# Kernel tuning notes

Measured on AMD Instinct MI355X. Metric: run time of the kernel, lower is better.

Reference implementation:

```python
import jax, jax.numpy as jnp
import numpy as np

B, LD, LP = 32, 512, 4096
DRUG_VOCAB, PROT_VOCAB, H = 600, 26, 128


def setup_inputs() -> dict:
    key = jax.random.key(0)
    ks = jax.random.split(key, 8)
    drug_ids = jax.random.randint(ks[0], (B, LD), 0, DRUG_VOCAB)
    prot_ids = jax.random.randint(ks[1], (B, LP), 0, PROT_VOCAB)
    drug_emb = jax.random.normal(ks[2], (DRUG_VOCAB, H), dtype=jnp.float32) * 0.02
    prot_emb = jax.random.normal(ks[3], (PROT_VOCAB, H), dtype=jnp.float32) * 0.02
    # classifier: Linear(2H -> 64), ReLU, Linear(64 -> 1); stored as [in, out]
    W1 = jax.random.normal(ks[4], (2 * H, 64), dtype=jnp.float32) * (1.0 / np.sqrt(2 * H))
    b1 = jnp.zeros((64,), dtype=jnp.float32)
    W2 = jax.random.normal(ks[5], (64, 1), dtype=jnp.float32) * (1.0 / np.sqrt(64))
    b2 = jnp.zeros((1,), dtype=jnp.float32)
    return {"drug_ids": drug_ids, "prot_ids": prot_ids,
            "drug_emb": drug_emb, "prot_emb": prot_emb,
            "W1": W1, "b1": b1, "W2": W2, "b2": b2}


def reference(drug_ids, prot_ids, drug_emb, prot_emb, W1, b1, W2, b2):
    d_feat = drug_emb[drug_ids]                      # [B, LD, H]
    p_feat = prot_emb[prot_ids]                      # [B, LP, H]
    aff = jnp.einsum('bld,bmd->blm', d_feat, p_feat) # [B, LD, LP]
    att_d = jax.nn.softmax(aff.max(axis=2), axis=1)[..., None]  # [B, LD, 1]
    att_p = jax.nn.softmax(aff.max(axis=1), axis=1)[..., None]  # [B, LP, 1]
    d_vec = (d_feat * att_d).sum(axis=1)             # [B, H]
    p_vec = (p_feat * att_p).sum(axis=1)             # [B, H]
    combined = jnp.concatenate([d_vec, p_vec], axis=1)  # [B, 2H]
    h = jax.nn.relu(combined @ W1 + b1)
    return h @ W2 + b2                               # [B, 1]
```

## Files before the change

### kernel.cpp

```cpp
#include <hip/hip_runtime.h>
#include <float.h>
#include <math.h>

#define NB 32
#define LD 512
#define LP 4096
#define HD 128
#define PV 26

__global__ __launch_bounds__(512) void k_scores(const int* __restrict__ drug_ids,
                                                const int* __restrict__ prot_ids,
                                                const float* __restrict__ drug_emb,
                                                const float* __restrict__ prot_emb,
                                                float* __restrict__ rowmax,
                                                float* __restrict__ colpart) {
    int b = blockIdx.x >> 3;
    int chunk = blockIdx.x & 7;
    int t = threadIdx.x;
    int q = __builtin_amdgcn_readfirstlane(t >> 6);
    int lane = t & 63;
    int l = chunk * 64 + lane;

    __shared__ float red[8][64][27];
    __shared__ unsigned wor[8];

    const int4* pid4 = reinterpret_cast<const int4*>(prot_ids + b * LP);
    int4 i0 = pid4[t], i1 = pid4[t + 512];
    unsigned pm = (1u << i0.x) | (1u << i0.y) | (1u << i0.z) | (1u << i0.w)
                | (1u << i1.x) | (1u << i1.y) | (1u << i1.z) | (1u << i1.w);
    #pragma unroll
    for (int off = 32; off; off >>= 1) pm |= __shfl_xor(pm, off, 64);
    if (lane == 0) wor[q] = pm;

    const float* __restrict__ A =
        drug_emb + (size_t)drug_ids[b * LD + l] * HD + q * 16;
    float4 a[4];
    #pragma unroll
    for (int i = 0; i < 4; ++i) a[i] = reinterpret_cast<const float4*>(A)[i];

    const float* __restrict__ Bq = prot_emb + q * 16;
    float s[PV];
    #pragma unroll
    for (int v = 0; v < PV; ++v) s[v] = 0.f;

    #pragma unroll
    for (int i = 0; i < 4; ++i) {
        float4 av = a[i];
        #pragma unroll
        for (int v = 0; v < PV; ++v) {
            float4 p = reinterpret_cast<const float4*>(Bq + v * HD)[i];
            s[v] = fmaf(av.x, p.x, fmaf(av.y, p.y,
                   fmaf(av.z, p.z, fmaf(av.w, p.w, s[v]))));
        }
    }

    #pragma unroll
    for (int v = 0; v < PV; ++v) red[q][lane][v] = s[v];
    __syncthreads();

    unsigned msk = wor[0] | wor[1] | wor[2] | wor[3]
                 | wor[4] | wor[5] | wor[6] | wor[7];

    for (int o = t; o < 64 * PV; o += 512) {
        int l2 = o / PV, v = o - l2 * PV;
        float sum = red[0][l2][v] + red[1][l2][v] + red[2][l2][v] + red[3][l2][v]
                  + red[4][l2][v] + red[5][l2][v] + red[6][l2][v] + red[7][l2][v];
        red[0][l2][v] = sum;
    }
    __syncthreads();

    if (t < 64) {
        float m = -FLT_MAX;
        #pragma unroll
        for (int v = 0; v < PV; ++v)
            if ((msk >> v) & 1) m = fmaxf(m, red[0][t][v]);
        rowmax[b * LD + chunk * 64 + t] = m;
    } else if (t < 64 + PV) {
        int v = t - 64;
        float m = -FLT_MAX;
        for (int r = 0; r < 64; ++r) m = fmaxf(m, red[0][r][v]);
        colpart[((b << 3) + chunk) * 32 + v] = m;
    }
}

__global__ __launch_bounds__(1024) void k_tail(const int* __restrict__ drug_ids,
                                               const int* __restrict__ prot_ids,
                                               const float* __restrict__ drug_emb,
                                               const float* __restrict__ prot_emb,
                                               const float* __restrict__ rowmax,
                                               const float* __restrict__ colpart,
                                               const float* __restrict__ W1,
                                               const float* __restrict__ b1,
                                               const float* __restrict__ W2,
                                               const float* __restrict__ b2,
                                               float* __restrict__ out) {
    int b = blockIdx.x;
    int t = threadIdx.x;
    int wid = t >> 6, lane = t & 63;

    __shared__ int   cnt4[4][PV];
    __shared__ int   scnt[PV];
    __shared__ int   sids[LD];
    __shared__ float att[LD];
    __shared__ float redm[8], reds[8];
    __shared__ float ew[PV];
    __shared__ float sInvP;
    __shared__ float comb[2 * HD];
    __shared__ float part[8][HD];
    __shared__ float hpart[4][64];

    float r = -FLT_MAX;
    if (t < LD) {
        sids[t] = drug_ids[b * LD + t];
        r = rowmax[b * LD + t];
    }
    float cm = -FLT_MAX;
    if (t >= LD && t < LD + PV) {
        int v = t - LD;
        #pragma unroll
        for (int c = 0; c < 8; ++c)
            cm = fmaxf(cm, colpart[((b << 3) + c) * 32 + v]);
    }
    if (t < 4 * PV) ((int*)cnt4)[t] = 0;
    __syncthreads();
    {
        int4 v = reinterpret_cast<const int4*>(prot_ids + b * LP)[t];
        int sub = wid & 3;
        atomicAdd(&cnt4[sub][v.x], 1);
        atomicAdd(&cnt4[sub][v.y], 1);
        atomicAdd(&cnt4[sub][v.z], 1);
        atomicAdd(&cnt4[sub][v.w], 1);
    }
    if (t < LD) {
        float m = r;
        #pragma unroll
        for (int off = 32; off; off >>= 1) m = fmaxf(m, __shfl_xor(m, off, 64));
        if (lane == 0) redm[wid] = m;
    }
    __syncthreads();
    if (t < PV) scnt[t] = cnt4[0][t] + cnt4[1][t] + cnt4[2][t] + cnt4[3][t];
    float gm = fmaxf(fmaxf(fmaxf(redm[0], redm[1]), fmaxf(redm[2], redm[3])),
                     fmaxf(fmaxf(redm[4], redm[5]), fmaxf(redm[6], redm[7])));
    if (t < LD) {
        float e = __expf(r - gm);
        att[t] = e;
        float ssum = e;
        #pragma unroll
        for (int off = 32; off; off >>= 1) ssum += __shfl_xor(ssum, off, 64);
        if (lane == 0) reds[wid] = ssum;
    }
    __syncthreads();
    float invD = 1.f / (reds[0] + reds[1] + reds[2] + reds[3] +
                        reds[4] + reds[5] + reds[6] + reds[7]);

    if (wid == 8) {
        int c = (lane < PV) ? scnt[lane] : 0;
        float m0 = (c > 0) ? cm : -FLT_MAX;
        float M = m0;
        #pragma unroll
        for (int off = 32; off; off >>= 1) M = fmaxf(M, __shfl_xor(M, off, 64));
        float w = (c > 0) ? (float)c * __expf(cm - M) : 0.f;
        float S = w;
        #pragma unroll
        for (int off = 32; off; off >>= 1) S += __shfl_xor(S, off, 64);
        if (lane < PV) ew[lane] = w;
        if (lane == 0) sInvP = 1.f / S;
    }

    {
        int h = t & 127, g = t >> 7;
        float acc = 0.f;
        #pragma unroll 8
        for (int i = 0; i < 64; ++i) {
            int l = g * 64 + i;
            acc = fmaf(att[l], drug_emb[(size_t)sids[l] * HD + h], acc);
        }
        part[g][h] = acc;
    }
    __syncthreads();

    if (t < HD) {
        float d = part[0][t] + part[1][t] + part[2][t] + part[3][t] +
                  part[4][t] + part[5][t] + part[6][t] + part[7][t];
        comb[t] = d * invD;
    } else if (t < 2 * HD) {
        int h = t - HD;
        float acc = 0.f;
        #pragma unroll
        for (int v = 0; v < PV; ++v)
            acc = fmaf(ew[v], prot_emb[v * HD + h], acc);
        comb[t] = acc * sInvP;
    }
    __syncthreads();

    if (t < 256) {
        int j = t & 63, seg = t >> 6;
        float acc = 0.f;
        #pragma unroll
        for (int k = 0; k < 64; ++k) {
            int kk = seg * 64 + k;
            acc = fmaf(comb[kk], W1[kk * 64 + j], acc);
        }
        hpart[seg][j] = acc;
    }
    __syncthreads();
    if (t < 64) {
        float hj = b1[t] + hpart[0][t] + hpart[1][t] + hpart[2][t] + hpart[3][t];
        hj = fmaxf(hj, 0.f);
        float o = hj * W2[t];
        #pragma unroll
        for (int off = 32; off; off >>= 1) o += __shfl_xor(o, off, 64);
        if (t == 0) out[b] = o + b2[0];
    }
}

extern "C" void kernel_launch(void* const* d_in, const int* in_sizes, int n_in,
                              void* d_out, int out_size, void* d_ws, size_t ws_size,
                              hipStream_t stream) {
    const int*   drug_ids = (const int*)d_in[0];
    const int*   prot_ids = (const int*)d_in[1];
    const float* drug_emb = (const float*)d_in[2];
    const float* prot_emb = (const float*)d_in[3];
    const float* W1 = (const float*)d_in[4];
    const float* b1 = (const float*)d_in[5];
    const float* W2 = (const float*)d_in[6];
    const float* b2 = (const float*)d_in[7];
    float* out = (float*)d_out;

    char* ws = (char*)d_ws;
    float* rowmax  = (float*)(ws + 0);
    float* colpart = (float*)(ws + 65536);

    k_scores<<<NB * 8, 512, 0, stream>>>(drug_ids, prot_ids, drug_emb, prot_emb,
                                         rowmax, colpart);
    k_tail<<<NB, 1024, 0, stream>>>(drug_ids, prot_ids, drug_emb, prot_emb,
                                    rowmax, colpart, W1, b1, W2, b2, out);
}
```

Before: 18.42 us.

## Fuse score and tail kernels via cooperative grid sync with split softmax

Merges the two kernels into one cooperative kernel with a grid-wide barrier. Each of the 256 blocks now computes a chunk-local softmax (max, denominator) and a partial attention-weighted drug vector plus a partial protein histogram, all written to workspace. After the grid sync, 32 blocks rescale and combine the partials, then run the MLP. This removes the second launch and the tail's serial 512-row gather in exchange for grid-sync cost and more workspace traffic.

```diff
diff --git a/kernel.cpp b/kernel.cpp
--- a/kernel.cpp
+++ b/kernel.cpp
@@ -1,6 +1,9 @@
 #include <hip/hip_runtime.h>
+#include <hip/hip_cooperative_groups.h>
 #include <float.h>
 #include <math.h>
+
+namespace cg = cooperative_groups;
 
 #define NB 32
 #define LD 512
@@ -8,188 +11,179 @@
 #define HD 128
 #define PV 26
 
-__global__ __launch_bounds__(512) void k_scores(const int* __restrict__ drug_ids,
-                                                const int* __restrict__ prot_ids,
-                                                const float* __restrict__ drug_emb,
-                                                const float* __restrict__ prot_emb,
-                                                float* __restrict__ rowmax,
-                                                float* __restrict__ colpart) {
-    int b = blockIdx.x >> 3;
-    int chunk = blockIdx.x & 7;
-    int t = threadIdx.x;
-    int q = __builtin_amdgcn_readfirstlane(t >> 6);
-    int lane = t & 63;
-    int l = chunk * 64 + lane;
-
-    __shared__ float red[8][64][27];
-    __shared__ unsigned wor[8];
-
-    const int4* pid4 = reinterpret_cast<const int4*>(prot_ids + b * LP);
-    int4 i0 = pid4[t], i1 = pid4[t + 512];
-    unsigned pm = (1u << i0.x) | (1u << i0.y) | (1u << i0.z) | (1u << i0.w)
-                | (1u << i1.x) | (1u << i1.y) | (1u << i1.z) | (1u << i1.w);
-    #pragma unroll
-    for (int off = 32; off; off >>= 1) pm |= __shfl_xor(pm, off, 64);
-    if (lane == 0) wor[q] = pm;
-
-    const float* __restrict__ A =
-        drug_emb + (size_t)drug_ids[b * LD + l] * HD + q * 16;
-    float4 a[4];
-    #pragma unroll
-    for (int i = 0; i < 4; ++i) a[i] = reinterpret_cast<const float4*>(A)[i];
-
-    const float* __restrict__ Bq = prot_emb + q * 16;
-    float s[PV];
-    #pragma unroll
-    for (int v = 0; v < PV; ++v) s[v] = 0.f;
-
-    #pragma unroll
-    for (int i = 0; i < 4; ++i) {
-        float4 av = a[i];
-        #pragma unroll
-        for (int v = 0; v < PV; ++v) {
-            float4 p = reinterpret_cast<const float4*>(Bq + v * HD)[i];
-            s[v] = fmaf(av.x, p.x, fmaf(av.y, p.y,
-                   fmaf(av.z, p.z, fmaf(av.w, p.w, s[v]))));
-        }
-    }
-
-    #pragma unroll
-    for (int v = 0; v < PV; ++v) red[q][lane][v] = s[v];
-    __syncthreads();
-
-    unsigned msk = wor[0] | wor[1] | wor[2] | wor[3]
-                 | wor[4] | wor[5] | wor[6] | wor[7];
-
-    for (int o = t; o < 64 * PV; o += 512) {
-        int l2 = o / PV, v = o - l2 * PV;
-        float sum = red[0][l2][v] + red[1][l2][v] + red[2][l2][v] + red[3][l2][v]
-                  + red[4][l2][v] + red[5][l2][v] + red[6][l2][v] + red[7][l2][v];
-        red[0][l2][v] = sum;
-    }
-    __syncthreads();
-
-    if (t < 64) {
-        float m = -FLT_MAX;
-        #pragma unroll
-        for (int v = 0; v < PV; ++v)
-            if ((msk >> v) & 1) m = fmaxf(m, red[0][t][v]);
-        rowmax[b * LD + chunk * 64 + t] = m;
-    } else if (t < 64 + PV) {
-        int v = t - 64;
-        float m = -FLT_MAX;
-        for (int r = 0; r < 64; ++r) m = fmaxf(m, red[0][r][v]);
-        colpart[((b << 3) + chunk) * 32 + v] = m;
-    }
-}
-
-__global__ __launch_bounds__(1024) void k_tail(const int* __restrict__ drug_ids,
-                                               const int* __restrict__ prot_ids,
-                                               const float* __restrict__ drug_emb,
-                                               const float* __restrict__ prot_emb,
-                                               const float* __restrict__ rowmax,
-                                               const float* __restrict__ colpart,
-                                               const float* __restrict__ W1,
-                                               const float* __restrict__ b1,
-                                               const float* __restrict__ W2,
-                                               const float* __restrict__ b2,
-                                               float* __restrict__ out) {
-    int b = blockIdx.x;
+__global__ __launch_bounds__(512)
+void k_fused(const int* __restrict__ drug_ids, const int* __restrict__ prot_ids,
+             const float* __restrict__ drug_emb, const float* __restrict__ prot_emb,
+             const float* __restrict__ W1, const float* __restrict__ b1,
+             const float* __restrict__ W2, const float* __restrict__ b2,
+             float* __restrict__ out, float* __restrict__ wsf) {
+    float* ws_m    = wsf;
+    float* ws_den  = wsf + 256;
+    float* ws_col  = wsf + 512;
+    float* ws_part = wsf + 8704;
+    int*   ws_hist = (int*)(wsf + 41472);
+
     int t = threadIdx.x;
     int wid = t >> 6, lane = t & 63;
 
-    __shared__ int   cnt4[4][PV];
-    __shared__ int   scnt[PV];
-    __shared__ int   sids[LD];
-    __shared__ float att[LD];
-    __shared__ float redm[8], reds[8];
-    __shared__ float ew[PV];
-    __shared__ float sInvP;
-    __shared__ float comb[2 * HD];
-    __shared__ float part[8][HD];
-    __shared__ float hpart[4][64];
-
-    float r = -FLT_MAX;
-    if (t < LD) {
-        sids[t] = drug_ids[b * LD + t];
-        r = rowmax[b * LD + t];
-    }
-    float cm = -FLT_MAX;
-    if (t >= LD && t < LD + PV) {
-        int v = t - LD;
-        #pragma unroll
-        for (int c = 0; c < 8; ++c)
-            cm = fmaxf(cm, colpart[((b << 3) + c) * 32 + v]);
-    }
-    if (t < 4 * PV) ((int*)cnt4)[t] = 0;
+    __shared__ float red[8][64][27];
+    __shared__ float ev[64];
+    __shared__ unsigned wor[8];
+    __shared__ int hist[32];
+
+    {
+        int b = blockIdx.x >> 3, chunk = blockIdx.x & 7;
+        int q = __builtin_amdgcn_readfirstlane(wid);
+        int l = chunk * 64 + lane;
+
+        if (t < 32) hist[t] = 0;
+
+        const int4* pid4 = reinterpret_cast<const int4*>(prot_ids + b * LP);
+        int4 i0 = pid4[t], i1 = pid4[t + 512];
+        unsigned pm = (1u << i0.x) | (1u << i0.y) | (1u << i0.z) | (1u << i0.w)
+                    | (1u << i1.x) | (1u << i1.y) | (1u << i1.z) | (1u << i1.w);
+        #pragma unroll
+        for (int off = 32; off; off >>= 1) pm |= __shfl_xor(pm, off, 64);
+        if (lane == 0) wor[q] = pm;
+
+        const float* __restrict__ A =
+            drug_emb + (size_t)drug_ids[b * LD + l] * HD + q * 16;
+        float4 a[4];
+        #pragma unroll
+        for (int i = 0; i < 4; ++i) a[i] = reinterpret_cast<const float4*>(A)[i];
+
+        __syncthreads();
+
+        atomicAdd(&hist[prot_ids[b * LP + chunk * 512 + t]], 1);
+
+        const float* __restrict__ Bq = prot_emb + q * 16;
+        float s[PV];
+        #pragma unroll
+        for (int v = 0; v < PV; ++v) s[v] = 0.f;
+        #pragma unroll
+        for (int i = 0; i < 4; ++i) {
+            float4 av = a[i];
+            #pragma unroll
+            for (int v = 0; v < PV; ++v) {
+                float4 p = reinterpret_cast<const float4*>(Bq + v * HD)[i];
+                s[v] = fmaf(av.x, p.x, fmaf(av.y, p.y,
+                       fmaf(av.z, p.z, fmaf(av.w, p.w, s[v]))));
+            }
+        }
+        #pragma unroll
+        for (int v = 0; v < PV; ++v) red[q][lane][v] = s[v];
+        __syncthreads();
+
+        unsigned msk = wor[0] | wor[1] | wor[2] | wor[3]
+                     | wor[4] | wor[5] | wor[6] | wor[7];
+
+        for (int o = t; o < 64 * PV; o += 512) {
+            int l2 = o / PV, v = o - l2 * PV;
+            red[0][l2][v] = red[0][l2][v] + red[1][l2][v] + red[2][l2][v]
+                          + red[3][l2][v] + red[4][l2][v] + red[5][l2][v]
+                          + red[6][l2][v] + red[7][l2][v];
+        }
+        __syncthreads();
+
+        if (wid == 0) {
+            float r = -FLT_MAX;
+            #pragma unroll
+            for (int v = 0; v < PV; ++v)
+                if ((msk >> v) & 1) r = fmaxf(r, red[0][lane][v]);
+            float m = r;
+            #pragma unroll
+            for (int off = 32; off; off >>= 1) m = fmaxf(m, __shfl_xor(m, off, 64));
+            float e = __expf(r - m);
+            ev[lane] = e;
+            float den = e;
+            #pragma unroll
+            for (int off = 32; off; off >>= 1) den += __shfl_xor(den, off, 64);
+            if (lane == 0) {
+                ws_m[(b << 3) + chunk] = m;
+                ws_den[(b << 3) + chunk] = den;
+            }
+        } else if (wid == 1 && lane < PV) {
+            float cmx = -FLT_MAX;
+            for (int r = 0; r < 64; ++r) cmx = fmaxf(cmx, red[0][r][lane]);
+            ws_col[((b << 3) + chunk) * 32 + lane] = cmx;
+        }
+        __syncthreads();
+
+        float myE = ev[lane];
+        #pragma unroll
+        for (int i = 0; i < 4; ++i) {
+            red[q][lane][4 * i + 0] = myE * a[i].x;
+            red[q][lane][4 * i + 1] = myE * a[i].y;
+            red[q][lane][4 * i + 2] = myE * a[i].z;
+            red[q][lane][4 * i + 3] = myE * a[i].w;
+        }
+        __syncthreads();
+
+        if (t < 128) {
+            int qq = t >> 4, c = t & 15;
+            float sum = 0.f;
+            for (int r = 0; r < 64; ++r) sum += red[qq][r][c];
+            ws_part[((b << 3) + chunk) * 128 + qq * 16 + c] = sum;
+        }
+        if (t < 32) ws_hist[((b << 3) + chunk) * 32 + t] = hist[t];
+    }
+
+    cg::this_grid().sync();
+
+    if (blockIdx.x >= NB) return;
+    int b = blockIdx.x;
+
+    __shared__ float sscale[8], ew[32], comb[2 * HD], hpart[4][64];
+    __shared__ float sInvD, sInvP;
+
+    if (t < 8) {
+        float m = ws_m[(b << 3) + t];
+        float M = m;
+        #pragma unroll
+        for (int off = 4; off; off >>= 1) M = fmaxf(M, __shfl_xor(M, off, 8));
+        float sc = __expf(m - M);
+        float dd = sc * ws_den[(b << 3) + t];
+        float D = dd;
+        #pragma unroll
+        for (int off = 4; off; off >>= 1) D += __shfl_xor(D, off, 8);
+        sscale[t] = sc;
+        if (t == 0) sInvD = 1.f / D;
+    } else if (wid == 1) {
+        int v = lane;
+        float cmx = -FLT_MAX; int c = 0;
+        if (v < PV) {
+            #pragma unroll
+            for (int c8 = 0; c8 < 8; ++c8) {
+                cmx = fmaxf(cmx, ws_col[((b << 3) + c8) * 32 + v]);
+                c += ws_hist[((b << 3) + c8) * 32 + v];
+            }
+        }
+        float m0 = (c > 0) ? cmx : -FLT_MAX;
+        float M2 = m0;
+        #pragma unroll
+        for (int off = 32; off; off >>= 1) M2 = fmaxf(M2, __shfl_xor(M2, off, 64));
+        float w = (c > 0) ? (float)c * __expf(cmx - M2) : 0.f;
+        float S = w;
+        #pragma unroll
+        for (int off = 32; off; off >>= 1) S += __shfl_xor(S, off, 64);
+        if (v < 32) ew[v] = (v < PV) ? w : 0.f;
+        if (lane == 0) sInvP = 1.f / S;
+    }
     __syncthreads();
-    {
-        int4 v = reinterpret_cast<const int4*>(prot_ids + b * LP)[t];
-        int sub = wid & 3;
-        atomicAdd(&cnt4[sub][v.x], 1);
-        atomicAdd(&cnt4[sub][v.y], 1);
-        atomicAdd(&cnt4[sub][v.z], 1);
-        atomicAdd(&cnt4[sub][v.w], 1);
-    }
-    if (t < LD) {
-        float m = r;
-        #pragma unroll
-        for (int off = 32; off; off >>= 1) m = fmaxf(m, __shfl_xor(m, off, 64));
-        if (lane == 0) redm[wid] = m;
-    }
-    __syncthreads();
-    if (t < PV) scnt[t] = cnt4[0][t] + cnt4[1][t] + cnt4[2][t] + cnt4[3][t];
-    float gm = fmaxf(fmaxf(fmaxf(redm[0], redm[1]), fmaxf(redm[2], redm[3])),
-                     fmaxf(fmaxf(redm[4], redm[5]), fmaxf(redm[6], redm[7])));
-    if (t < LD) {
-        float e = __expf(r - gm);
-        att[t] = e;
-        float ssum = e;
-        #pragma unroll
-        for (int off = 32; off; off >>= 1) ssum += __shfl_xor(ssum, off, 64);
-        if (lane == 0) reds[wid] = ssum;
-    }
-    __syncthreads();
-    float invD = 1.f / (reds[0] + reds[1] + reds[2] + reds[3] +
-                        reds[4] + reds[5] + reds[6] + reds[7]);
-
-    if (wid == 8) {
-        int c = (lane < PV) ? scnt[lane] : 0;
-        float m0 = (c > 0) ? cm : -FLT_MAX;
-        float M = m0;
-        #pragma unroll
-        for (int off = 32; off; off >>= 1) M = fmaxf(M, __shfl_xor(M, off, 64));
-        float w = (c > 0) ? (float)c * __expf(cm - M) : 0.f;
-        float S = w;
-        #pragma unroll
-        for (int off = 32; off; off >>= 1) S += __shfl_xor(S, off, 64);
-        if (lane < PV) ew[lane] = w;
-        if (lane == 0) sInvP = 1.f / S;
-    }
-
-    {
-        int h = t & 127, g = t >> 7;
-        float acc = 0.f;
-        #pragma unroll 8
-        for (int i = 0; i < 64; ++i) {
-            int l = g * 64 + i;
-            acc = fmaf(att[l], drug_emb[(size_t)sids[l] * HD + h], acc);
-        }
-        part[g][h] = acc;
-    }
-    __syncthreads();
 
     if (t < HD) {
-        float d = part[0][t] + part[1][t] + part[2][t] + part[3][t] +
-                  part[4][t] + part[5][t] + part[6][t] + part[7][t];
-        comb[t] = d * invD;
+        float d = 0.f;
+        #pragma unroll
+        for (int c8 = 0; c8 < 8; ++c8)
+            d = fmaf(sscale[c8], ws_part[((b << 3) + c8) * 128 + t], d);
+        comb[t] = d * sInvD;
     } else if (t < 2 * HD) {
         int h = t - HD;
-        float acc = 0.f;
+        float p = 0.f;
         #pragma unroll
         for (int v = 0; v < PV; ++v)
-            acc = fmaf(ew[v], prot_emb[v * HD + h], acc);
-        comb[t] = acc * sInvP;
+            p = fmaf(ew[v], prot_emb[v * HD + h], p);
+        comb[t] = p * sInvP;
     }
     __syncthreads();
 
@@ -226,13 +220,11 @@
     const float* W2 = (const float*)d_in[6];
     const float* b2 = (const float*)d_in[7];
     float* out = (float*)d_out;
-
-    char* ws = (char*)d_ws;
-    float* rowmax  = (float*)(ws + 0);
-    float* colpart = (float*)(ws + 65536);
-
-    k_scores<<<NB * 8, 512, 0, stream>>>(drug_ids, prot_ids, drug_emb, prot_emb,
-                                         rowmax, colpart);
-    k_tail<<<NB, 1024, 0, stream>>>(drug_ids, prot_ids, drug_emb, prot_emb,
-                                    rowmax, colpart, W1, b1, W2, b2, out);
+    float* wsf = (float*)d_ws;
+
+    void* kargs[] = { (void*)&drug_ids, (void*)&prot_ids, (void*)&drug_emb,
+                      (void*)&prot_emb, (void*)&W1, (void*)&b1, (void*)&W2,
+                      (void*)&b2, (void*)&out, (void*)&wsf };
+    hipLaunchCooperativeKernel((void*)k_fused, dim3(NB * 8), dim3(512),
+                               kargs, 0, stream);
 }
```

Measured after the change: 52.14 us. 183% more time.
